# Kernel tuning notes

Measured on AMD Instinct MI355X. Metric: run time of the kernel, lower is better.

Reference implementation:

```python
import jax, jax.numpy as jnp
import numpy as np

B, S, D = 4, 2048, 512
H, DK, DV = 8, 64, 64
EPS = 1e-6
MASK_FILL = -1e-9  # faithful to the original masked_fill value (NOT -inf)


def setup_inputs() -> dict:
    key = jax.random.key(0)
    ks = jax.random.split(key, 9)
    sc = 0.05
    return {
        "q": jax.random.normal(ks[0], (B, S, D), jnp.float32),
        "k": jax.random.normal(ks[1], (B, S, D), jnp.float32),
        "v": jax.random.normal(ks[2], (B, S, D), jnp.float32),
        "src_mask": jax.random.randint(ks[3], (B, S), 0, 2, jnp.int32),
        "Wq": jax.random.normal(ks[4], (D, H * DK), jnp.float32) * sc,
        "Wk": jax.random.normal(ks[5], (D, H * DK), jnp.float32) * sc,
        "Wv": jax.random.normal(ks[6], (D, H * DV), jnp.float32) * sc,
        "Wo": jax.random.normal(ks[7], (H * DV, D), jnp.float32) * sc,
        "gamma": jnp.ones((D,), jnp.float32),
        "beta": jnp.zeros((D,), jnp.float32),
    }


def reference(q, k, v, src_mask, Wq, Wk, Wv, Wo, gamma, beta):
    b, len_q, _ = q.shape
    residual = q
    # QKV projections -> [B, H, S, dk/dv]
    qh = (q @ Wq).reshape(b, len_q, H, DK).transpose(0, 2, 1, 3)
    kh = (k @ Wk).reshape(b, -1, H, DK).transpose(0, 2, 1, 3)
    vh = (v @ Wv).reshape(b, -1, H, DV).transpose(0, 2, 1, 3)
    # scores [B, H, S, S]
    attn = jnp.einsum('bhqd,bhkd->bhqk', qh, kh) / jnp.sqrt(jnp.float32(DK))
    # pairwise src mask: outer product of [B,S] mask, diagonal forced to 1
    sm = src_mask[:, :len_q].astype(jnp.float32)
    am = sm[:, :, None] * sm[:, None, :]               # [B, S, S]
    idx = jnp.arange(len_q)
    am = am.at[:, idx, idx].set(1.0)
    attn = jnp.where(am[:, None, :, :] == 0, MASK_FILL, attn)
    attn = jax.nn.softmax(attn, axis=-1)
    out = jnp.einsum('bhqk,bhkd->bhqd', attn, vh)      # [B, H, S, dv]
    out = out.transpose(0, 2, 1, 3).reshape(b, len_q, H * DV)
    out = out @ Wo + residual
    # LayerNorm(eps=1e-6)
    mu = jnp.mean(out, axis=-1, keepdims=True)
    var = jnp.var(out, axis=-1, keepdims=True)
    out = (out - mu) * jax.lax.rsqrt(var + EPS) * gamma + beta
    return out, attn
```

## Files before the change

kernel.cpp:

```cpp
#include <hip/hip_runtime.h>
#include <math.h>

#define B_ 4
#define S_ 2048
#define D_ 512
#define H_ 8
#define NEG_FILL (-1e-9f)

typedef __attribute__((ext_vector_type(8))) short bf16x8;
typedef __attribute__((ext_vector_type(4))) float f32x4;

#define MFMA16(A, Bm, C) __builtin_amdgcn_mfma_f32_16x16x32_bf16((A), (Bm), (C), 0, 0, 0)

__device__ __forceinline__ short f2b(float f) {
  union { float f; unsigned u; } x;
  x.f = f;
  unsigned r = x.u + 0x7fffu + ((x.u >> 16) & 1u);
  return (short)(r >> 16);
}

__global__ __launch_bounds__(256) void prep_wt(
    const float* __restrict__ Wq, const float* __restrict__ Wk,
    const float* __restrict__ Wv, const float* __restrict__ Wo,
    short* __restrict__ Wqt, short* __restrict__ Wkt,
    short* __restrict__ Wvt, short* __restrict__ Wot)
{
  const float* W; short* Wt;
  switch (blockIdx.z) {
    case 0: W = Wq; Wt = Wqt; break;
    case 1: W = Wk; Wt = Wkt; break;
    case 2: W = Wv; Wt = Wvt; break;
    default: W = Wo; Wt = Wot; break;
  }
  __shared__ float Ws[64 * 68];
  const int t = threadIdx.x;
  const int n0 = blockIdx.x * 64, k0 = blockIdx.y * 64;

  #pragma unroll
  for (int rep = 0; rep < 4; ++rep) {
    int e4 = rep * 256 + t;
    int r = e4 >> 4, c0 = (e4 & 15) * 4;
    *(float4*)&Ws[r * 68 + c0] = *(const float4*)&W[(size_t)(k0 + r) * 512 + n0 + c0];
  }
  __syncthreads();

  int rn = t >> 2;
  int kb = (t & 3) * 16;
  union { short s[8]; int4 v; } pk;
  #pragma unroll
  for (int half = 0; half < 2; ++half) {
    #pragma unroll
    for (int i = 0; i < 8; ++i)
      pk.s[i] = f2b(Ws[(kb + half * 8 + i) * 68 + rn]);
    *(int4*)&Wt[(size_t)(n0 + rn) * 512 + k0 + kb + half * 8] = pk.v;
  }
}

__global__ __launch_bounds__(256) void qkv_mfma(
    const float* __restrict__ q, const float* __restrict__ k, const float* __restrict__ v,
    const short* __restrict__ Wqt, const short* __restrict__ Wkt, const short* __restrict__ Wvt,
    short* __restrict__ qh, short* __restrict__ kh, short* __restrict__ vt)
{
  const int z = blockIdx.z;
  const float* X = (z == 0) ? q : (z == 1) ? k : v;
  const short* Wt = (z == 0) ? Wqt : (z == 1) ? Wkt : Wvt;

  __shared__ short Xs[64 * 72];
  __shared__ short Wsh[64 * 72];

  const int t = threadIdx.x;
  const int wave = t >> 6, lane = t & 63, quad = lane >> 4, l15 = lane & 15;
  const int tile_n = blockIdx.x * 64;
  const int tile_m = blockIdx.y * 64;

  f32x4 acc[4];
  #pragma unroll
  for (int nt = 0; nt < 4; ++nt) acc[nt] = (f32x4){0.f, 0.f, 0.f, 0.f};

  for (int k0 = 0; k0 < 512; k0 += 64) {
    __syncthreads();
    #pragma unroll
    for (int rep = 0; rep < 4; ++rep) {
      int e4 = rep * 256 + t;
      int row = e4 >> 4, c0 = (e4 & 15) * 4;
      float4 xv = *(const float4*)&X[(size_t)(tile_m + row) * 512 + k0 + c0];
      *(short4*)&Xs[row * 72 + c0] =
          make_short4(f2b(xv.x), f2b(xv.y), f2b(xv.z), f2b(xv.w));
    }
    #pragma unroll
    for (int rep = 0; rep < 2; ++rep) {
      int e = rep * 256 + t;
      int row = e >> 3, c0 = (e & 7) * 8;
      *(int4*)&Wsh[row * 72 + c0] = *(const int4*)&Wt[(size_t)(tile_n + row) * 512 + k0 + c0];
    }
    __syncthreads();
    #pragma unroll
    for (int ks = 0; ks < 2; ++ks) {
      bf16x8 af = *(bf16x8*)&Xs[(wave * 16 + l15) * 72 + ks * 32 + quad * 8];
      #pragma unroll
      for (int nt = 0; nt < 4; ++nt) {
        bf16x8 bfr = *(bf16x8*)&Wsh[(nt * 16 + l15) * 72 + ks * 32 + quad * 8];
        acc[nt] = MFMA16(af, bfr, acc[nt]);
      }
    }
  }

  const int h = tile_n >> 6;
  if (z < 2) {
    short* Y = (z == 0) ? qh : kh;
    #pragma unroll
    for (int nt = 0; nt < 4; ++nt) {
      int d = nt * 16 + l15;
      #pragma unroll
      for (int r = 0; r < 4; ++r) {
        int row = tile_m + wave * 16 + quad * 4 + r;
        int b = row >> 11, s = row & (S_ - 1);
        Y[(((size_t)(b * H_ + h)) * S_ + s) * 64 + d] = f2b(acc[nt][r]);
      }
    }
  } else {
    int row0 = tile_m + wave * 16 + quad * 4;
    int b = row0 >> 11, s0 = row0 & (S_ - 1);
    #pragma unroll
    for (int nt = 0; nt < 4; ++nt) {
      int d = nt * 16 + l15;
      short4 pk = make_short4(f2b(acc[nt][0]), f2b(acc[nt][1]),
                              f2b(acc[nt][2]), f2b(acc[nt][3]));
      *(short4*)&vt[(((size_t)(b * H_ + h)) * 64 + d) * S_ + s0] = pk;
    }
  }
}

__global__ __launch_bounds__(256) void attn_mfma(
    const short* __restrict__ qh, const short* __restrict__ kh,
    const short* __restrict__ vt, const int* __restrict__ src_mask,
    float* __restrict__ attn_out, short* __restrict__ ohb)
{
  const int t = threadIdx.x;
  const int wave = t >> 6, lane = t & 63, quad = lane >> 4, l15 = lane & 15;
  const int q0 = blockIdx.x * 64;
  const int bh = blockIdx.y, b = bh >> 3, h = bh & 7;

  __shared__ short Ks[64 * 72];
  __shared__ short Vs[64 * 72];
  __shared__ short Ps[64 * 72];
  __shared__ int smq[64], smk[64];

  #pragma unroll
  for (int rep = 0; rep < 2; ++rep) {
    int e = rep * 256 + t;
    int row = e >> 3, c0 = (e & 7) * 8;
    *(int4*)&Ps[row * 72 + c0] =
        *(const int4*)&qh[((size_t)bh * S_ + q0 + row) * 64 + c0];
  }
  if (t < 64) smq[t] = src_mask[b * S_ + q0 + t];
  __syncthreads();

  bf16x8 qf[2];
  #pragma unroll
  for (int ks = 0; ks < 2; ++ks)
    qf[ks] = *(bf16x8*)&Ps[(wave * 16 + l15) * 72 + ks * 32 + quad * 8];

  int rloc[4], mqr[4], qir[4];
  #pragma unroll
  for (int r = 0; r < 4; ++r) {
    rloc[r] = wave * 16 + quad * 4 + r;
    mqr[r] = smq[rloc[r]];
    qir[r] = q0 + rloc[r];
  }

  float rs[4] = {0.f, 0.f, 0.f, 0.f};
  for (int kt0 = 0; kt0 < S_; kt0 += 64) {
    __syncthreads();
    #pragma unroll
    for (int rep = 0; rep < 2; ++rep) {
      int e = rep * 256 + t;
      int row = e >> 3, c0 = (e & 7) * 8;
      *(int4*)&Ks[row * 72 + c0] =
          *(const int4*)&kh[((size_t)bh * S_ + kt0 + row) * 64 + c0];
    }
    if (t < 64) smk[t] = src_mask[b * S_ + kt0 + t];
    __syncthreads();

    #pragma unroll
    for (int nt = 0; nt < 4; ++nt) {
      f32x4 c = (f32x4){0.f, 0.f, 0.f, 0.f};
      #pragma unroll
      for (int ks = 0; ks < 2; ++ks) {
        bf16x8 kf = *(bf16x8*)&Ks[(nt * 16 + l15) * 72 + ks * 32 + quad * 8];
        c = MFMA16(qf[ks], kf, c);
      }
      int mk = smk[nt * 16 + l15];
      int kj = kt0 + nt * 16 + l15;
      #pragma unroll
      for (int r = 0; r < 4; ++r) {
        float ss = c[r] * 0.125f;
        bool keep = (mqr[r] & mk) || (qir[r] == kj);
        ss = keep ? ss : NEG_FILL;
        rs[r] += __expf(ss);
      }
    }
  }
  #pragma unroll
  for (int r = 0; r < 4; ++r) {
    float vsum = rs[r];
    vsum += __shfl_xor(vsum, 1);
    vsum += __shfl_xor(vsum, 2);
    vsum += __shfl_xor(vsum, 4);
    vsum += __shfl_xor(vsum, 8);
    rs[r] = 1.f / vsum;
  }

  f32x4 oacc[4];
  #pragma unroll
  for (int dt = 0; dt < 4; ++dt) oacc[dt] = (f32x4){0.f, 0.f, 0.f, 0.f};

  for (int kt0 = 0; kt0 < S_; kt0 += 64) {
    __syncthreads();
    #pragma unroll
    for (int rep = 0; rep < 2; ++rep) {
      int e = rep * 256 + t;
      int row = e >> 3, c0 = (e & 7) * 8;
      *(int4*)&Ks[row * 72 + c0] =
          *(const int4*)&kh[((size_t)bh * S_ + kt0 + row) * 64 + c0];
      *(int4*)&Vs[row * 72 + c0] =
          *(const int4*)&vt[((size_t)bh * 64 + row) * S_ + kt0 + c0];
    }
    if (t < 64) smk[t] = src_mask[b * S_ + kt0 + t];
    __syncthreads();

    #pragma unroll
    for (int nt = 0; nt < 4; ++nt) {
      f32x4 c = (f32x4){0.f, 0.f, 0.f, 0.f};
      #pragma unroll
      for (int ks = 0; ks < 2; ++ks) {
        bf16x8 kf = *(bf16x8*)&Ks[(nt * 16 + l15) * 72 + ks * 32 + quad * 8];
        c = MFMA16(qf[ks], kf, c);
      }
      int mk = smk[nt * 16 + l15];
      int kj = kt0 + nt * 16 + l15;
      #pragma unroll
      for (int r = 0; r < 4; ++r) {
        float ss = c[r] * 0.125f;
        bool keep = (mqr[r] & mk) || (qir[r] == kj);
        ss = keep ? ss : NEG_FILL;
        float p = __expf(ss) * rs[r];
        attn_out[((size_t)bh * S_ + q0 + rloc[r]) * S_ + kj] = p;
        Ps[rloc[r] * 72 + nt * 16 + l15] = f2b(p);
      }
    }
    __syncthreads();

    bf16x8 pf[2];
    #pragma unroll
    for (int ks = 0; ks < 2; ++ks)
      pf[ks] = *(bf16x8*)&Ps[(wave * 16 + l15) * 72 + ks * 32 + quad * 8];
    #pragma unroll
    for (int dt = 0; dt < 4; ++dt) {
      #pragma unroll
      for (int ks = 0; ks < 2; ++ks) {
        bf16x8 vf = *(bf16x8*)&Vs[(dt * 16 + l15) * 72 + ks * 32 + quad * 8];
        oacc[dt] = MFMA16(pf[ks], vf, oacc[dt]);
      }
    }
  }

  #pragma unroll
  for (int dt = 0; dt < 4; ++dt) {
    int d = h * 64 + dt * 16 + l15;
    #pragma unroll
    for (int r = 0; r < 4; ++r)
      ohb[((size_t)b * S_ + q0 + rloc[r]) * 512 + d] = f2b(oacc[dt][r]);
  }
}

__global__ __launch_bounds__(256) void out_mfma(
    const short* __restrict__ ohb, const short* __restrict__ Wot,
    const float* __restrict__ resid, float* __restrict__ out)
{
  __shared__ short Xs[64 * 72];
  __shared__ short Wsh[64 * 72];

  const int t = threadIdx.x;
  const int wave = t >> 6, lane = t & 63, quad = lane >> 4, l15 = lane & 15;
  const int tile_n = blockIdx.x * 64;
  const int tile_m = blockIdx.y * 64;

  f32x4 acc[4];
  #pragma unroll
  for (int nt = 0; nt < 4; ++nt) acc[nt] = (f32x4){0.f, 0.f, 0.f, 0.f};

  for (int k0 = 0; k0 < 512; k0 += 64) {
    __syncthreads();
    #pragma unroll
    for (int rep = 0; rep < 2; ++rep) {
      int e = rep * 256 + t;
      int row = e >> 3, c0 = (e & 7) * 8;
      *(int4*)&Xs[row * 72 + c0] = *(const int4*)&ohb[(size_t)(tile_m + row) * 512 + k0 + c0];
      *(int4*)&Wsh[row * 72 + c0] = *(const int4*)&Wot[(size_t)(tile_n + row) * 512 + k0 + c0];
    }
    __syncthreads();
    #pragma unroll
    for (int ks = 0; ks < 2; ++ks) {
      bf16x8 af = *(bf16x8*)&Xs[(wave * 16 + l15) * 72 + ks * 32 + quad * 8];
      #pragma unroll
      for (int nt = 0; nt < 4; ++nt) {
        bf16x8 bfr = *(bf16x8*)&Wsh[(nt * 16 + l15) * 72 + ks * 32 + quad * 8];
        acc[nt] = MFMA16(af, bfr, acc[nt]);
      }
    }
  }

  #pragma unroll
  for (int nt = 0; nt < 4; ++nt) {
    int c = tile_n + nt * 16 + l15;
    #pragma unroll
    for (int r = 0; r < 4; ++r) {
      size_t row = tile_m + wave * 16 + quad * 4 + r;
      out[row * 512 + c] = acc[nt][r] + resid[row * 512 + c];
    }
  }
}

__global__ __launch_bounds__(256) void ln_kernel(
    float* __restrict__ io, const float* __restrict__ gamma, const float* __restrict__ beta)
{
  const int wid  = threadIdx.x >> 6;
  const int lane = threadIdx.x & 63;
  const size_t row = (size_t)blockIdx.x * 4 + wid;
  const size_t base = row * 512 + lane * 8;

  float4 x0 = *(const float4*)&io[base];
  float4 x1 = *(const float4*)&io[base + 4];
  float xs[8] = {x0.x, x0.y, x0.z, x0.w, x1.x, x1.y, x1.z, x1.w};

  float s = 0.f, s2 = 0.f;
  #pragma unroll
  for (int i = 0; i < 8; ++i) { s += xs[i]; s2 = fmaf(xs[i], xs[i], s2); }
  #pragma unroll
  for (int m = 1; m < 64; m <<= 1) {
    s  += __shfl_xor(s, m);
    s2 += __shfl_xor(s2, m);
  }
  float mu  = s * (1.f / 512.f);
  float var = s2 * (1.f / 512.f) - mu * mu;
  float rsq = rsqrtf(var + 1e-6f);

  float4 g0 = *(const float4*)&gamma[lane * 8];
  float4 g1 = *(const float4*)&gamma[lane * 8 + 4];
  float4 b0 = *(const float4*)&beta[lane * 8];
  float4 b1 = *(const float4*)&beta[lane * 8 + 4];
  float gs[8] = {g0.x, g0.y, g0.z, g0.w, g1.x, g1.y, g1.z, g1.w};
  float bs[8] = {b0.x, b0.y, b0.z, b0.w, b1.x, b1.y, b1.z, b1.w};

  float ys[8];
  #pragma unroll
  for (int i = 0; i < 8; ++i) ys[i] = (xs[i] - mu) * rsq * gs[i] + bs[i];
  *(float4*)&io[base]     = make_float4(ys[0], ys[1], ys[2], ys[3]);
  *(float4*)&io[base + 4] = make_float4(ys[4], ys[5], ys[6], ys[7]);
}

extern "C" void kernel_launch(void* const* d_in, const int* in_sizes, int n_in,
                              void* d_out, int out_size, void* d_ws, size_t ws_size,
                              hipStream_t stream)
{
  const float* q     = (const float*)d_in[0];
  const float* k     = (const float*)d_in[1];
  const float* v     = (const float*)d_in[2];
  const int*  smask  = (const int*)d_in[3];
  const float* Wq    = (const float*)d_in[4];
  const float* Wk    = (const float*)d_in[5];
  const float* Wv    = (const float*)d_in[6];
  const float* Wo    = (const float*)d_in[7];
  const float* gamma = (const float*)d_in[8];
  const float* beta  = (const float*)d_in[9];

  float* out  = (float*)d_out;
  float* attn = out + (size_t)B_ * S_ * D_;

  short* wsS = (short*)d_ws;
  short* qh  = wsS;
  short* kh  = qh + 4194304;
  short* vt  = kh + 4194304;
  short* ohb = vt + 4194304;
  short* Wqt = ohb + 4194304;
  short* Wkt = Wqt + 262144;
  short* Wvt = Wkt + 262144;
  short* Wot = Wvt + 262144;

  prep_wt<<<dim3(8, 8, 4), 256, 0, stream>>>(Wq, Wk, Wv, Wo, Wqt, Wkt, Wvt, Wot);
  qkv_mfma<<<dim3(8, 128, 3), 256, 0, stream>>>(q, k, v, Wqt, Wkt, Wvt, qh, kh, vt);
  attn_mfma<<<dim3(32, 32), 256, 0, stream>>>(qh, kh, vt, smask, attn, ohb);
  out_mfma<<<dim3(8, 128), 256, 0, stream>>>(ohb, Wot, q, out);
  ln_kernel<<<2048, 256, 0, stream>>>(out, gamma, beta);
}
```

Before: 807.3 us.

## Load K/V fragments directly from global, drop block syncs, remap blocks for L2 locality

The attention kernel stops staging K and V tiles through shared memory. Each wave now reads its MFMA fragments straight from global memory, keeps a private per-wave P tile in LDS, and preloads the whole batch mask row once. This removes the block-wide __syncthreads pairs in both passes. Blocks are also remapped so that neighbouring launches share a (b,h) slice, which should improve L2 reuse of K and V. The cost is more redundant global and L2 traffic, since four waves each load the same K/V fragments without coalesced staging.

```diff
diff --git a/kernel.cpp b/kernel.cpp
--- a/kernel.cpp
+++ b/kernel.cpp
@@ -138,60 +138,49 @@
 {
   const int t = threadIdx.x;
   const int wave = t >> 6, lane = t & 63, quad = lane >> 4, l15 = lane & 15;
-  const int q0 = blockIdx.x * 64;
-  const int bh = blockIdx.y, b = bh >> 3, h = bh & 7;
-
-  __shared__ short Ks[64 * 72];
-  __shared__ short Vs[64 * 72];
-  __shared__ short Ps[64 * 72];
-  __shared__ int smq[64], smk[64];
+
+  const int lin = blockIdx.y * 32 + blockIdx.x;
+  const int nl  = (lin & 7) * 128 + (lin >> 3);
+  const int bh = nl >> 5, b = bh >> 3, h = bh & 7;
+  const int q0 = (nl & 31) * 64;
+
+  __shared__ short Ps[4][16 * 72];
+  __shared__ int smAll[S_];
 
   #pragma unroll
   for (int rep = 0; rep < 2; ++rep) {
-    int e = rep * 256 + t;
-    int row = e >> 3, c0 = (e & 7) * 8;
-    *(int4*)&Ps[row * 72 + c0] =
-        *(const int4*)&qh[((size_t)bh * S_ + q0 + row) * 64 + c0];
-  }
-  if (t < 64) smq[t] = src_mask[b * S_ + q0 + t];
+    int idx = (rep * 256 + t) * 4;
+    *(int4*)&smAll[idx] = *(const int4*)&src_mask[b * S_ + idx];
+  }
   __syncthreads();
 
-  bf16x8 qf[2];
-  #pragma unroll
-  for (int ks = 0; ks < 2; ++ks)
-    qf[ks] = *(bf16x8*)&Ps[(wave * 16 + l15) * 72 + ks * 32 + quad * 8];
+  const short* __restrict__ khb = kh + (size_t)bh * S_ * 64;
+  const short* __restrict__ vtb = vt + (size_t)bh * 64 * S_;
+
+  const size_t qrow = (size_t)bh * S_ + q0 + wave * 16 + l15;
+  const bf16x8 qf0 = *(const bf16x8*)&qh[qrow * 64 + quad * 8];
+  const bf16x8 qf1 = *(const bf16x8*)&qh[qrow * 64 + 32 + quad * 8];
 
   int rloc[4], mqr[4], qir[4];
   #pragma unroll
   for (int r = 0; r < 4; ++r) {
     rloc[r] = wave * 16 + quad * 4 + r;
-    mqr[r] = smq[rloc[r]];
     qir[r] = q0 + rloc[r];
+    mqr[r] = smAll[qir[r]];
   }
 
   float rs[4] = {0.f, 0.f, 0.f, 0.f};
   for (int kt0 = 0; kt0 < S_; kt0 += 64) {
-    __syncthreads();
-    #pragma unroll
-    for (int rep = 0; rep < 2; ++rep) {
-      int e = rep * 256 + t;
-      int row = e >> 3, c0 = (e & 7) * 8;
-      *(int4*)&Ks[row * 72 + c0] =
-          *(const int4*)&kh[((size_t)bh * S_ + kt0 + row) * 64 + c0];
-    }
-    if (t < 64) smk[t] = src_mask[b * S_ + kt0 + t];
-    __syncthreads();
-
     #pragma unroll
     for (int nt = 0; nt < 4; ++nt) {
+      const short* kp = khb + (size_t)(kt0 + nt * 16 + l15) * 64 + quad * 8;
+      bf16x8 kf0 = *(const bf16x8*)kp;
+      bf16x8 kf1 = *(const bf16x8*)(kp + 32);
       f32x4 c = (f32x4){0.f, 0.f, 0.f, 0.f};
-      #pragma unroll
-      for (int ks = 0; ks < 2; ++ks) {
-        bf16x8 kf = *(bf16x8*)&Ks[(nt * 16 + l15) * 72 + ks * 32 + quad * 8];
-        c = MFMA16(qf[ks], kf, c);
-      }
-      int mk = smk[nt * 16 + l15];
+      c = MFMA16(qf0, kf0, c);
+      c = MFMA16(qf1, kf1, c);
       int kj = kt0 + nt * 16 + l15;
+      int mk = smAll[kj];
       #pragma unroll
       for (int r = 0; r < 4; ++r) {
         float ss = c[r] * 0.125f;
@@ -215,53 +204,42 @@
   #pragma unroll
   for (int dt = 0; dt < 4; ++dt) oacc[dt] = (f32x4){0.f, 0.f, 0.f, 0.f};
 
+  short* __restrict__ ps = Ps[wave];
+  float* __restrict__ arow[4];
+  #pragma unroll
+  for (int r = 0; r < 4; ++r)
+    arow[r] = attn_out + ((size_t)bh * S_ + q0 + rloc[r]) * S_;
+
   for (int kt0 = 0; kt0 < S_; kt0 += 64) {
-    __syncthreads();
-    #pragma unroll
-    for (int rep = 0; rep < 2; ++rep) {
-      int e = rep * 256 + t;
-      int row = e >> 3, c0 = (e & 7) * 8;
-      *(int4*)&Ks[row * 72 + c0] =
-          *(const int4*)&kh[((size_t)bh * S_ + kt0 + row) * 64 + c0];
-      *(int4*)&Vs[row * 72 + c0] =
-          *(const int4*)&vt[((size_t)bh * 64 + row) * S_ + kt0 + c0];
-    }
-    if (t < 64) smk[t] = src_mask[b * S_ + kt0 + t];
-    __syncthreads();
-
     #pragma unroll
     for (int nt = 0; nt < 4; ++nt) {
+      const short* kp = khb + (size_t)(kt0 + nt * 16 + l15) * 64 + quad * 8;
+      bf16x8 kf0 = *(const bf16x8*)kp;
+      bf16x8 kf1 = *(const bf16x8*)(kp + 32);
       f32x4 c = (f32x4){0.f, 0.f, 0.f, 0.f};
-      #pragma unroll
-      for (int ks = 0; ks < 2; ++ks) {
-        bf16x8 kf = *(bf16x8*)&Ks[(nt * 16 + l15) * 72 + ks * 32 + quad * 8];
-        c = MFMA16(qf[ks], kf, c);
-      }
-      int mk = smk[nt * 16 + l15];
+      c = MFMA16(qf0, kf0, c);
+      c = MFMA16(qf1, kf1, c);
       int kj = kt0 + nt * 16 + l15;
+      int mk = smAll[kj];
       #pragma unroll
       for (int r = 0; r < 4; ++r) {
         float ss = c[r] * 0.125f;
         bool keep = (mqr[r] & mk) || (qir[r] == kj);
         ss = keep ? ss : NEG_FILL;
         float p = __expf(ss) * rs[r];
-        attn_out[((size_t)bh * S_ + q0 + rloc[r]) * S_ + kj] = p;
-        Ps[rloc[r] * 72 + nt * 16 + l15] = f2b(p);
-      }
-    }
-    __syncthreads();
-
-    bf16x8 pf[2];
-    #pragma unroll
-    for (int ks = 0; ks < 2; ++ks)
-      pf[ks] = *(bf16x8*)&Ps[(wave * 16 + l15) * 72 + ks * 32 + quad * 8];
+        arow[r][kj] = p;
+        ps[(quad * 4 + r) * 72 + nt * 16 + l15] = f2b(p);
+      }
+    }
+    bf16x8 pf0 = *(bf16x8*)&ps[l15 * 72 + quad * 8];
+    bf16x8 pf1 = *(bf16x8*)&ps[l15 * 72 + 32 + quad * 8];
     #pragma unroll
     for (int dt = 0; dt < 4; ++dt) {
-      #pragma unroll
-      for (int ks = 0; ks < 2; ++ks) {
-        bf16x8 vf = *(bf16x8*)&Vs[(dt * 16 + l15) * 72 + ks * 32 + quad * 8];
-        oacc[dt] = MFMA16(pf[ks], vf, oacc[dt]);
-      }
+      const short* vp = vtb + (size_t)(dt * 16 + l15) * S_ + kt0 + quad * 8;
+      bf16x8 vf0 = *(const bf16x8*)vp;
+      bf16x8 vf1 = *(const bf16x8*)(vp + 32);
+      oacc[dt] = MFMA16(pf0, vf0, oacc[dt]);
+      oacc[dt] = MFMA16(pf1, vf1, oacc[dt]);
     }
   }
 
```

Result: slower. 976.0 us (+20.9%).
